# Performance work log

Hardware: AMD Instinct MI355X
Metric: run time of the kernel (lower is better)

Reference implementation:

```python
import jax, jax.numpy as jnp
import numpy as np

B = 8192

def setup_inputs() -> dict:
    key = jax.random.key(0)
    k1, k2, k3 = jax.random.split(key, 3)
    z = jax.random.normal(k1, (B, 1), dtype=jnp.float32)
    censorship = jax.random.bernoulli(k2, 0.5, (B,)).astype(jnp.float32)
    times = jax.random.uniform(k3, (B,), dtype=jnp.float32) * 100.0
    c_t = jnp.stack([censorship, times], axis=1)  # (B, 2)
    return {"z": z, "c_t": c_t}

def reference(z, c_t):
    # phi='sigmoid', reduction='mean'
    censorship = c_t[:, 0]
    times = c_t[:, 1]
    events = 1.0 - censorship  # 1 if event observed
    zf = z[:, 0]  # (B,)
    # pair (a,b) comparable iff time_a < time_b and event_a observed;
    # then a is more risky, b less risky -> r = z_a - z_b
    comparable = (times[:, None] < times[None, :]) & (events[:, None] > 0)  # (B,B)
    r = zf[:, None] - zf[None, :]  # (B,B)
    vals = jnp.where(comparable, jax.nn.sigmoid(r), 0.0)
    n_pairs = jnp.sum(comparable)
    total = jnp.sum(vals)
    # mean over comparable pairs; return 0 if none (matches torch.zeros(1) fallback)
    loss = -jnp.where(n_pairs > 0, total / jnp.maximum(n_pairs, 1).astype(vals.dtype), 0.0)
    return loss
```

## Files before the change

### kernel.cpp

```cpp
#include <hip/hip_runtime.h>


constexpr int THREADS = 256;
constexpr int JT = 256;

__global__ __launch_bounds__(256) void surv_pairs(
    const float* __restrict__ z, const float* __restrict__ ct,
    float2* __restrict__ P, int njc)
{
    __shared__ float s_t[JT];
    __shared__ float s_e[JT];
    __shared__ float s_tg[THREADS];
    __shared__ float s_ei[THREADS];
    __shared__ int   s_wcnt[4];

    const int tid = threadIdx.x;
    const int ib  = blockIdx.x / njc;
    const int jc  = blockIdx.x % njc;
    const int j0  = jc * JT;

    {
        const int j = j0 + tid;
        s_t[tid] = ct[2 * j + 1];
        s_e[tid] = __expf(z[j]);
    }

    const int i = ib * THREADS + tid;
    const float cens = ct[2 * i];
    const float ti   = ct[2 * i + 1];
    const float eii  = __expf(z[i]);
    const bool  ev   = (1.0f - cens) > 0.0f;
    const unsigned long long mask = __ballot(ev);
    const int lane = tid & 63;
    const int wid  = tid >> 6;
    if (lane == 0) s_wcnt[wid] = __popcll(mask);
    __syncthreads();
    int base = 0;
    for (int w = 0; w < wid; ++w) base += s_wcnt[w];
    const int m = s_wcnt[0] + s_wcnt[1] + s_wcnt[2] + s_wcnt[3];
    const int pos = base + __popcll(mask & ((1ull << lane) - 1ull));
    if (ev) { s_tg[pos] = ti; s_ei[pos] = eii; }
    __syncthreads();

    const bool act = tid < m;
    float tg = 0.0f, ei = 0.0f;
    if (act) { tg = s_tg[tid]; ei = s_ei[tid]; }

    float fsum = 0.0f;
    int   cnt  = 0;
    if (act) {
        const float4* t4 = reinterpret_cast<const float4*>(s_t);
        const float4* e4 = reinterpret_cast<const float4*>(s_e);
#pragma unroll 8
        for (int q = 0; q < JT / 4; ++q) {
            const float4 t = t4[q];
            const float4 e = e4[q];
            { bool c = tg < t.x; float sg = ei * __builtin_amdgcn_rcpf(ei + e.x); fsum += c ? sg : 0.0f; cnt += c; }
            { bool c = tg < t.y; float sg = ei * __builtin_amdgcn_rcpf(ei + e.y); fsum += c ? sg : 0.0f; cnt += c; }
            { bool c = tg < t.z; float sg = ei * __builtin_amdgcn_rcpf(ei + e.z); fsum += c ? sg : 0.0f; cnt += c; }
            { bool c = tg < t.w; float sg = ei * __builtin_amdgcn_rcpf(ei + e.w); fsum += c ? sg : 0.0f; cnt += c; }
        }
    }

    for (int off = 32; off > 0; off >>= 1) {
        fsum += __shfl_down(fsum, off);
        cnt  += __shfl_down(cnt, off);
    }
    __shared__ float wsum[4];
    __shared__ int   wcnt2[4];
    if (lane == 0) { wsum[wid] = fsum; wcnt2[wid] = cnt; }
    __syncthreads();
    if (tid == 0) {
        const float bs = wsum[0] + wsum[1] + wsum[2] + wsum[3];
        const int   bc = wcnt2[0] + wcnt2[1] + wcnt2[2] + wcnt2[3];
        P[blockIdx.x] = make_float2(bs, (float)bc);
    }
}

__global__ __launch_bounds__(256) void surv_fin(
    const float2* __restrict__ P, int nb, float* __restrict__ out)
{
    const int tid = threadIdx.x;
    double s = 0.0, c = 0.0;
    for (int k = tid; k < nb; k += THREADS) {
        const float2 p = P[k];
        s += p.x; c += p.y;
    }
    __shared__ double ss[THREADS];
    __shared__ double sc[THREADS];
    ss[tid] = s; sc[tid] = c;
    __syncthreads();
    for (int off = THREADS / 2; off > 0; off >>= 1) {
        if (tid < off) { ss[tid] += ss[tid + off]; sc[tid] += sc[tid + off]; }
        __syncthreads();
    }
    if (tid == 0) {
        const double n = sc[0];
        out[0] = (n > 0.0) ? (float)(-(ss[0] / n)) : 0.0f;
    }
}

extern "C" void kernel_launch(void* const* d_in, const int* in_sizes, int n_in,
                              void* d_out, int out_size, void* d_ws, size_t ws_size,
                              hipStream_t stream)
{
    const float* z  = (const float*)d_in[0];
    const float* ct = (const float*)d_in[1];
    float* out = (float*)d_out;
    const int B = in_sizes[0];

    const int NB  = B / THREADS;
    const int njc = B / JT;

    float2* P = (float2*)d_ws;

    surv_pairs<<<NB * njc, THREADS, 0, stream>>>(z, ct, P, njc);
    surv_fin<<<1, THREADS, 0, stream>>>(P, NB * njc, out);
}
```

Measured before the change: 20.85 us.

## Rotate compacted event rows across wavefronts and simplify sigmoid to fma+rcp

Rewrites the sigmoid as 1/(1+e_j*exp(-z_i)), so each term costs one FMA plus one reciprocal instead of an add, a reciprocal and a multiply. Compacted event rows are assigned to wavefronts in a chunk order rotated by block index. Wavefronts whose chunk holds no events skip the whole loop, and the skipping wavefronts are spread across SIMD positions instead of always being the last ones. The finalize kernel is shrunk to a single wavefront using shuffle reductions, which removes the shared-memory tree and its barriers.

```diff
diff --git a/kernel.cpp b/kernel.cpp
--- a/kernel.cpp
+++ b/kernel.cpp
@@ -11,8 +11,10 @@
     __shared__ float s_t[JT];
     __shared__ float s_e[JT];
     __shared__ float s_tg[THREADS];
-    __shared__ float s_ei[THREADS];
+    __shared__ float s_ri[THREADS];
     __shared__ int   s_wcnt[4];
+    __shared__ float wsum[4];
+    __shared__ int   wcnt2[4];
 
     const int tid = threadIdx.x;
     const int ib  = blockIdx.x / njc;
@@ -28,7 +30,7 @@
     const int i = ib * THREADS + tid;
     const float cens = ct[2 * i];
     const float ti   = ct[2 * i + 1];
-    const float eii  = __expf(z[i]);
+    const float rii  = __expf(-z[i]);
     const bool  ev   = (1.0f - cens) > 0.0f;
     const unsigned long long mask = __ballot(ev);
     const int lane = tid & 63;
@@ -39,26 +41,28 @@
     for (int w = 0; w < wid; ++w) base += s_wcnt[w];
     const int m = s_wcnt[0] + s_wcnt[1] + s_wcnt[2] + s_wcnt[3];
     const int pos = base + __popcll(mask & ((1ull << lane) - 1ull));
-    if (ev) { s_tg[pos] = ti; s_ei[pos] = eii; }
+    if (ev) { s_tg[pos] = ti; s_ri[pos] = rii; }
     __syncthreads();
 
-    const bool act = tid < m;
-    float tg = 0.0f, ei = 0.0f;
-    if (act) { tg = s_tg[tid]; ei = s_ei[tid]; }
+    const int chunk = (wid + (int)blockIdx.x) & 3;
+    const int row   = chunk * 64 + lane;
+    const bool act  = row < m;
+    const float tg = act ? s_tg[row] : __builtin_inff();
+    const float ri = act ? s_ri[row] : 0.0f;
 
     float fsum = 0.0f;
     int   cnt  = 0;
-    if (act) {
+    if (chunk * 64 < m) {
         const float4* t4 = reinterpret_cast<const float4*>(s_t);
         const float4* e4 = reinterpret_cast<const float4*>(s_e);
 #pragma unroll 8
         for (int q = 0; q < JT / 4; ++q) {
             const float4 t = t4[q];
             const float4 e = e4[q];
-            { bool c = tg < t.x; float sg = ei * __builtin_amdgcn_rcpf(ei + e.x); fsum += c ? sg : 0.0f; cnt += c; }
-            { bool c = tg < t.y; float sg = ei * __builtin_amdgcn_rcpf(ei + e.y); fsum += c ? sg : 0.0f; cnt += c; }
-            { bool c = tg < t.z; float sg = ei * __builtin_amdgcn_rcpf(ei + e.z); fsum += c ? sg : 0.0f; cnt += c; }
-            { bool c = tg < t.w; float sg = ei * __builtin_amdgcn_rcpf(ei + e.w); fsum += c ? sg : 0.0f; cnt += c; }
+            { bool c = tg < t.x; float d = __builtin_fmaf(e.x, ri, 1.0f); float s = __builtin_amdgcn_rcpf(d); fsum += c ? s : 0.0f; cnt += c; }
+            { bool c = tg < t.y; float d = __builtin_fmaf(e.y, ri, 1.0f); float s = __builtin_amdgcn_rcpf(d); fsum += c ? s : 0.0f; cnt += c; }
+            { bool c = tg < t.z; float d = __builtin_fmaf(e.z, ri, 1.0f); float s = __builtin_amdgcn_rcpf(d); fsum += c ? s : 0.0f; cnt += c; }
+            { bool c = tg < t.w; float d = __builtin_fmaf(e.w, ri, 1.0f); float s = __builtin_amdgcn_rcpf(d); fsum += c ? s : 0.0f; cnt += c; }
         }
     }
 
@@ -66,8 +70,6 @@
         fsum += __shfl_down(fsum, off);
         cnt  += __shfl_down(cnt, off);
     }
-    __shared__ float wsum[4];
-    __shared__ int   wcnt2[4];
     if (lane == 0) { wsum[wid] = fsum; wcnt2[wid] = cnt; }
     __syncthreads();
     if (tid == 0) {
@@ -77,27 +79,21 @@
     }
 }
 
-__global__ __launch_bounds__(256) void surv_fin(
+__global__ __launch_bounds__(64) void surv_fin(
     const float2* __restrict__ P, int nb, float* __restrict__ out)
 {
-    const int tid = threadIdx.x;
+    const int lane = threadIdx.x;
     double s = 0.0, c = 0.0;
-    for (int k = tid; k < nb; k += THREADS) {
+    for (int k = lane; k < nb; k += 64) {
         const float2 p = P[k];
         s += p.x; c += p.y;
     }
-    __shared__ double ss[THREADS];
-    __shared__ double sc[THREADS];
-    ss[tid] = s; sc[tid] = c;
-    __syncthreads();
-    for (int off = THREADS / 2; off > 0; off >>= 1) {
-        if (tid < off) { ss[tid] += ss[tid + off]; sc[tid] += sc[tid + off]; }
-        __syncthreads();
+    for (int off = 32; off > 0; off >>= 1) {
+        s += __shfl_down(s, off);
+        c += __shfl_down(c, off);
     }
-    if (tid == 0) {
-        const double n = sc[0];
-        out[0] = (n > 0.0) ? (float)(-(ss[0] / n)) : 0.0f;
-    }
+    if (lane == 0)
+        out[0] = (c > 0.0) ? (float)(-(s / c)) : 0.0f;
 }
 
 extern "C" void kernel_launch(void* const* d_in, const int* in_sizes, int n_in,
@@ -115,5 +111,5 @@
     float2* P = (float2*)d_ws;
 
     surv_pairs<<<NB * njc, THREADS, 0, stream>>>(z, ct, P, njc);
-    surv_fin<<<1, THREADS, 0, stream>>>(P, NB * njc, out);
+    surv_fin<<<1, 64, 0, stream>>>(P, NB * njc, out);
 }
```

Measured after the change: 21.38 us. 2.5% more time.
